# Optimization experiments

Measured on AMD Instinct MI355X. Metric: run time of the kernel, lower is better.

Reference implementation:

```python
import jax, jax.numpy as jnp
import numpy as np

EPS = 1e-5
AVG_D = 32.0


def setup_inputs() -> dict:
    key = jax.random.key(0)
    ks = jax.random.split(key, 12)
    Ns, Nd, E, D, K = 1_000_000, 100_000, 3_200_000, 16, 2
    Fs, Fd, V = 4, 4, 100_000
    F = Fd + K  # predictor fields
    inp = {}
    inp["Cat_src"] = jax.random.randint(ks[0], (Ns, Fs), 0, V)
    inp["Cat_dst"] = jax.random.randint(ks[1], (Nd, Fd), 0, V)
    inp["src_ids"] = jax.random.randint(ks[2], (E,), 0, Ns)
    inp["dst_ids"] = jax.random.randint(ks[3], (E,), 0, Nd)
    inp["label"] = jax.random.randint(ks[4], (Nd,), 0, 2)
    inp["w"] = jax.random.normal(ks[5], (V, D), dtype=jnp.float32) * 0.05
    inp["W_agg"] = jax.random.normal(ks[6], (K, 12 * D, D), dtype=jnp.float32) * 0.05
    inp["b_agg"] = jnp.zeros((K, D), jnp.float32)
    inp["w_lin"] = jax.random.normal(ks[7], (F * D,), dtype=jnp.float32) * 0.05
    inp["b_lin"] = jnp.zeros((1,), jnp.float32)
    inp["W1"] = jax.random.normal(ks[8], (F * D, 64), dtype=jnp.float32) * 0.05
    inp["b1"] = jnp.zeros((64,), jnp.float32)
    inp["W2"] = jax.random.normal(ks[9], (64, 32), dtype=jnp.float32) * 0.05
    inp["b2"] = jnp.zeros((32,), jnp.float32)
    inp["W3"] = jax.random.normal(ks[10], (32, 1), dtype=jnp.float32) * 0.05
    inp["b3"] = jnp.zeros((1,), jnp.float32)
    return inp


def reference(Cat_src, Cat_dst, src_ids, dst_ids, label, w, W_agg, b_agg,
              w_lin, b_lin, W1, b1, W2, b2, W3, b3):
    Nd = Cat_dst.shape[0]
    # --- node embedding: gather cat fields, RowEmb with modes [mean, max] -> [Ns, K, D]
    emb = w[Cat_src]                                      # [Ns, Fs, D]
    h_src = jnp.stack([emb.mean(1), emb.max(1)], axis=1)  # [Ns, K, D]
    # --- multi-aggregator message passing (copy_u + segment min/max/mean, std via mean of h^2)
    m = h_src[src_ids]                                    # [E, K, D]
    deg = jax.ops.segment_sum(jnp.ones(src_ids.shape, m.dtype), dst_ids, Nd)
    safe = jnp.maximum(deg, 1.0)[:, None, None]
    mean = jax.ops.segment_sum(m, dst_ids, Nd) / safe
    mean2 = jax.ops.segment_sum(m * m, dst_ids, Nd) / safe
    has = (deg > 0)[:, None, None]
    mn = jnp.where(has, jax.ops.segment_min(m, dst_ids, Nd), 0.0)
    mx = jnp.where(has, jax.ops.segment_max(m, dst_ids, Nd), 0.0)
    std = jnp.sqrt(jax.nn.relu(mean2 - mean * mean) + EPS)
    tmp = jnp.concatenate([mean, mn, mx, std], axis=-1)   # [Nd, K, 4D]
    # --- PNA degree scalers: identity / amplification / attenuation
    logd = jnp.log(deg + 1.0)
    log_avg = jnp.log(AVG_D + 1.0)
    amp = (logd / log_avg)[:, None, None]
    att = jnp.where(logd > 0, log_avg / jnp.maximum(logd, EPS), 0.0)[:, None, None]
    scaled = jnp.concatenate([tmp, tmp * amp, tmp * att], axis=-1)  # [Nd, K, 12D]
    mes = jnp.einsum('nkf,kfd->nkd', scaled, W_agg) + b_agg          # [Nd, K, D]
    # --- final block: concat dst cat embeddings with aggregated messages
    x = jnp.concatenate([w[Cat_dst], mes], axis=1)        # [Nd, F, D]
    # --- DeepFM predictor: linear + FM pairwise + deep MLP
    flat = x.reshape(Nd, -1)
    lin = flat @ w_lin + b_lin[0]
    s = x.sum(1)
    fm = 0.5 * ((s * s) - (x * x).sum(1)).sum(-1)
    h = jax.nn.relu(flat @ W1 + b1)
    h = jax.nn.relu(h @ W2 + b2)
    deep = (h @ W3 + b3)[:, 0]
    pred = jax.nn.sigmoid(lin + fm + deep)
    return (pred, label)
```

## Files before the change

### kernel.cpp

```cpp
#include <hip/hip_runtime.h>
#include <math.h>

#define EPSF 1e-5f
#define BSH  5
#define BSZ  32
#define MAXB 4096
#define SBH  9
#define MAXSB 256
#define TILE 4096
#define SEG  8
#define BCAP 1472
#define SBCAP (16 * BCAP)
#define XPADS2 104
#define X2PADS 72
#define NPACK 14336

typedef __attribute__((ext_vector_type(8))) short short8;
typedef __attribute__((ext_vector_type(4))) float float4v;

__device__ inline unsigned f2bf_rne(float x) {
    unsigned u = __float_as_uint(x);
    u += 0x7FFF + ((u >> 16) & 1);
    return u >> 16;
}
__device__ inline short bf16_of(float x) { return (short)f2bf_rne(x); }
__device__ inline float bf2f_lo(unsigned hv) { return __uint_as_float(hv << 16); }
__device__ inline float bf2f_hi(unsigned hv) { return __uint_as_float(hv & 0xFFFF0000u); }
__device__ inline float bf2f_s(ushort s) { return __uint_as_float((unsigned)s << 16); }

__global__ __launch_bounds__(256) void setup_all(
    int* sbcursor, int* gcur, int nb, int nsb,
    const float* __restrict__ W_agg, const float* __restrict__ W1,
    const float* __restrict__ W2, ushort* __restrict__ wpack,
    const float* __restrict__ w, ushort* __restrict__ wb, int VD, int do_cast)
{
    int nzc = (nb + 255) >> 8;
    int bid = blockIdx.x;
    if (bid < nzc) {
        int i = bid * 256 + threadIdx.x;
        if (i < nb) gcur[i] = i * BCAP;
        if (i < nsb) sbcursor[i] = i * SBCAP;
        return;
    }
    if (bid == nzc) {
        for (int it = threadIdx.x; it < 1792; it += 256) {
            if (it < 768) {
                int t_g = it >> 6; int rem = it & 63;
                int q = rem >> 4, col = rem & 15;
                int kvar = t_g / 6, t = t_g % 6;
                const float* src = W_agg + kvar * 3072 + (t * 32 + q * 8) * 16 + col;
                ushort* dst = wpack + (size_t)it * 8;
#pragma unroll
                for (int j = 0; j < 8; ++j) dst[j] = (ushort)f2bf_rne(src[j * 16]);
            } else if (it < 1536) {
                int i2 = it - 768;
                int t = i2 >> 8; int rem = i2 & 255;
                int q = rem >> 6, col = rem & 63;
                const float* src = W1 + (t * 32 + q * 8) * 64 + col;
                ushort* dst = wpack + 6144 + (size_t)i2 * 8;
#pragma unroll
                for (int j = 0; j < 8; ++j) dst[j] = (ushort)f2bf_rne(src[j * 64]);
            } else {
                int i2 = it - 1536;
                int t = i2 >> 7; int rem = i2 & 127;
                int q = rem >> 5, col = rem & 31;
                const float* src = W2 + (t * 32 + q * 8) * 32 + col;
                ushort* dst = wpack + 12288 + (size_t)i2 * 8;
#pragma unroll
                for (int j = 0; j < 8; ++j) dst[j] = (ushort)f2bf_rne(src[j * 32]);
            }
        }
        return;
    }
    if (!do_cast) return;
    int i4 = ((bid - nzc - 1) * 256 + threadIdx.x) * 4;
    if (i4 + 3 < VD) {
        float4 v = *(const float4*)(w + i4);
        ushort4 o;
        o.x = (ushort)f2bf_rne(v.x); o.y = (ushort)f2bf_rne(v.y);
        o.z = (ushort)f2bf_rne(v.z); o.w = (ushort)f2bf_rne(v.w);
        *(ushort4*)(wb + i4) = o;
    } else {
        for (int j = i4; j < VD; ++j) wb[j] = (ushort)f2bf_rne(w[j]);
    }
}

__global__ __launch_bounds__(256) void build_h(
    const int* __restrict__ Cat_src, const ushort* __restrict__ wb,
    unsigned* __restrict__ h, int Ns)
{
    int gid = blockIdx.x * 256 + threadIdx.x;
    int s = gid >> 4;
    if (s >= Ns) return;
    int lane = threadIdx.x & 63;
    int d = lane & 15;
    int c = Cat_src[s * 4 + (d & 3)];
    float vs = 0.f, vm = -INFINITY;
#pragma unroll
    for (int f = 0; f < 4; ++f) {
        int id = __shfl(c, (lane & 48) + f, 64);
        float a = bf2f_s(wb[id * 16 + d]);
        vs += a; vm = fmaxf(vm, a);
    }
    unsigned packed = f2bf_rne(vs * 0.25f) | (f2bf_rne(vm) << 16);
    __builtin_nontemporal_store(packed, &h[s * 16 + d]);
}

__global__ __launch_bounds__(256) void scatter_sb(
    const int* __restrict__ src_ids, const int* __restrict__ dst_ids,
    int* sbcursor, unsigned* __restrict__ pairs1, int E, int nsb)
{
    __shared__ int cnt[MAXSB];
    __shared__ int base[MAXSB];
    int tid = threadIdx.x;
    int t0 = blockIdx.x * TILE;
    for (int i = tid; i < nsb; i += 256) cnt[i] = 0;
    __syncthreads();
    int rank[TILE / 256];
#pragma unroll
    for (int j = 0; j < TILE / 256; ++j) {
        int e = t0 + j * 256 + tid;
        rank[j] = (e < E) ? atomicAdd(&cnt[dst_ids[e] >> SBH], 1) : 0;
    }
    __syncthreads();
    for (int i = tid; i < nsb; i += 256) {
        int c = cnt[i];
        base[i] = c ? atomicAdd(&sbcursor[i], c) : 0;
    }
    __syncthreads();
#pragma unroll
    for (int j = 0; j < TILE / 256; ++j) {
        int e = t0 + j * 256 + tid;
        if (e < E) {
            int d = dst_ids[e];
            int sb = d >> SBH;
            int idx = base[sb] + rank[j];
            if (idx < (sb + 1) * SBCAP)
                pairs1[idx] = ((unsigned)src_ids[e] << 9) | (unsigned)(d & 511);
        }
    }
}

__global__ __launch_bounds__(256) void scatter_fine(
    const unsigned* __restrict__ pairs1, const int* __restrict__ sbcursor,
    int* gcur, unsigned* __restrict__ pairs2, int nb, int nsb)
{
    __shared__ int cnt[16];
    __shared__ int base[16];
    int S = blockIdx.x >> 3, seg = blockIdx.x & (SEG - 1);
    int tid = threadIdx.x;
    int sbs = S * SBCAP;
    int sbe = sbcursor[S];
    if (sbe > sbs + SBCAP) sbe = sbs + SBCAP;
    int len = sbe - sbs;
    int per = (len + SEG - 1) / SEG;
    int s0 = sbs + seg * per;
    int s1 = s0 + per; if (s1 > sbe) s1 = sbe;
    if (tid < 16) cnt[tid] = 0;
    __syncthreads();
    int rank[12];
    unsigned pv[12];
    int nit = (s1 - s0 + 255) >> 8;
    if (nit > 12) nit = 12;
    for (int j = 0; j < nit; ++j) {
        int e = s0 + j * 256 + tid;
        if (e < s1) {
            unsigned p = __builtin_nontemporal_load(&pairs1[e]);
            pv[j] = p;
            rank[j] = atomicAdd(&cnt[(p >> 5) & 15], 1);
        }
    }
    __syncthreads();
    if (tid < 16) {
        int gb = (S << 4) + tid;
        int c = cnt[tid];
        base[tid] = (c && gb < nb) ? atomicAdd(&gcur[gb], c) : 0;
    }
    __syncthreads();
    for (int j = 0; j < nit; ++j) {
        int e = s0 + j * 256 + tid;
        if (e < s1) {
            unsigned p = pv[j];
            int fb = (p >> 5) & 15;
            int gb = (S << 4) + fb;
            int idx = base[fb] + rank[j];
            if (idx < (gb + 1) * BCAP)
                pairs2[idx] = p;
        }
    }
}


__device__ inline void bucket_sort(const unsigned* __restrict__ pairs,
                                   int gbase, int cnt,
                                   unsigned* sp, int* hist, int* ofs, int* start,
                                   int tid)
{
    if (tid < BSZ) hist[tid] = 0;
    __syncthreads();
    for (int i = tid; i < cnt; i += 256)
        atomicAdd(&hist[__builtin_nontemporal_load(&pairs[gbase + i]) & (BSZ - 1)], 1);
    __syncthreads();
    if (tid < BSZ) ofs[tid] = hist[tid];
    __syncthreads();
    for (int off = 1; off < BSZ; off <<= 1) {
        int y = (tid < BSZ && tid >= off) ? ofs[tid - off] : 0;
        __syncthreads();
        if (tid < BSZ) ofs[tid] += y;
        __syncthreads();
    }
    if (tid < BSZ) {
        start[tid] = ofs[tid] - hist[tid];
        ofs[tid] = ofs[tid] - hist[tid];
    }
    __syncthreads();
    for (int i = tid; i < cnt; i += 256) {
        unsigned p = __builtin_nontemporal_load(&pairs[gbase + i]);
        int r = atomicAdd(&ofs[p & (BSZ - 1)], 1);
        sp[r] = p;
    }
    __syncthreads();
}

__device__ inline void emit_stats(float sum0, float sq0, float mn0, float mx0,
                                  float sum1, float sq1, float mn1, float mx1,
                                  int dg, int n, int lane, int sub,
                                  ushort* __restrict__ tmpb, int* __restrict__ deg_out)
{
#pragma unroll
    for (int off = 16; off <= 32; off <<= 1) {
        sum0 += __shfl_xor(sum0, off); sq0 += __shfl_xor(sq0, off);
        mn0 = fminf(mn0, __shfl_xor(mn0, off)); mx0 = fmaxf(mx0, __shfl_xor(mx0, off));
        sum1 += __shfl_xor(sum1, off); sq1 += __shfl_xor(sq1, off);
        mn1 = fminf(mn1, __shfl_xor(mn1, off)); mx1 = fmaxf(mx1, __shfl_xor(mx1, off));
    }
    float safe = fmaxf((float)dg, 1.f);
    float r = 1.f / safe;
    bool has = dg > 0;
    float mean0 = sum0 * r, mean1 = sum1 * r;
    float sd0 = sqrtf(fmaxf(sq0 * r - mean0 * mean0, 0.f) + EPSF);
    float sd1 = sqrtf(fmaxf(sq1 * r - mean1 * mean1, 0.f) + EPSF);
    float v0 = (sub == 0) ? mean0 : (sub == 1) ? (has ? mn0 : 0.f)
             : (sub == 2) ? (has ? mx0 : 0.f) : sd0;
    float v1 = (sub == 0) ? mean1 : (sub == 1) ? (has ? mn1 : 0.f)
             : (sub == 2) ? (has ? mx1 : 0.f) : sd1;
    ushort* tp = tmpb + (size_t)n * 128;
    tp[lane] = (ushort)f2bf_rne(v0);
    tp[64 + lane] = (ushort)f2bf_rne(v1);
    if (lane == 0) deg_out[n] = dg;
}

__global__ __launch_bounds__(256) void agg_from_h(
    const unsigned* __restrict__ h, const int* __restrict__ gcur,
    const unsigned* __restrict__ pairs,
    ushort* __restrict__ tmpb, int* __restrict__ deg_out, int Nd)
{
    __shared__ unsigned sp[BCAP];
    __shared__ int hist[BSZ];
    __shared__ int ofs[BSZ];
    __shared__ int start[BSZ];
    int b = blockIdx.x, tid = threadIdx.x;
    int gbase = b * BCAP;
    int cnt = gcur[b] - gbase;
    if (cnt > BCAP) cnt = BCAP;
    if (cnt < 0) cnt = 0;
    bucket_sort(pairs, gbase, cnt, sp, hist, ofs, start, tid);

    int wv = tid >> 6, lane = tid & 63, sub = lane >> 4, d = lane & 15;
#pragma unroll 1
    for (int q = 0; q < 8; ++q) {
        int dl = wv * 8 + q;
        int n = b * BSZ + dl;
        if (n >= Nd) break;
        int st = start[dl], dg = hist[dl];
        float sum0 = 0.f, sq0 = 0.f, mn0 = INFINITY, mx0 = -INFINITY;
        float sum1 = 0.f, sq1 = 0.f, mn1 = INFINITY, mx1 = -INFINITY;
        int nt = (dg + 31) >> 5;
        for (int t = 0; t < nt; ++t) {
            int base = t * 32 + sub;
            unsigned hv[8];
#pragma unroll
            for (int j = 0; j < 8; ++j) {
                int e = base + j * 4;
                int ec = (e < dg) ? e : (dg - 1);
                unsigned p = sp[st + ec];
                hv[j] = h[(p >> 9) * 16 + d];
            }
#pragma unroll
            for (int j = 0; j < 8; ++j) {
                int e = base + j * 4;
                if (e < dg) {
                    float me = bf2f_lo(hv[j]);
                    float vm = bf2f_hi(hv[j]);
                    sum0 += me; sq0 += me * me;
                    mn0 = fminf(mn0, me); mx0 = fmaxf(mx0, me);
                    sum1 += vm; sq1 += vm * vm;
                    mn1 = fminf(mn1, vm); mx1 = fmaxf(mx1, vm);
                }
            }
        }
        emit_stats(sum0, sq0, mn0, mx0, sum1, sq1, mn1, mx1,
                   dg, n, lane, sub, tmpb, deg_out);
    }
}

__global__ __launch_bounds__(256) void agg_from_w(
    const int* __restrict__ Cat_src, const float* __restrict__ w,
    const ushort* __restrict__ wb, int use_bf, const int* __restrict__ gcur,
    const unsigned* __restrict__ pairs,
    ushort* __restrict__ tmpb, int* __restrict__ deg_out, int Nd)
{
    __shared__ unsigned sp[BCAP];
    __shared__ int hist[BSZ];
    __shared__ int ofs[BSZ];
    __shared__ int start[BSZ];
    int b = blockIdx.x, tid = threadIdx.x;
    int gbase = b * BCAP;
    int cnt = gcur[b] - gbase;
    if (cnt > BCAP) cnt = BCAP;
    if (cnt < 0) cnt = 0;
    bucket_sort(pairs, gbase, cnt, sp, hist, ofs, start, tid);

    int wv = tid >> 6, lane = tid & 63, sub = lane >> 4, d = lane & 15;
#pragma unroll 1
    for (int q = 0; q < 8; ++q) {
        int dl = wv * 8 + q;
        int n = b * BSZ + dl;
        if (n >= Nd) break;
        int st = start[dl], dg = hist[dl];
        float sum0 = 0.f, sq0 = 0.f, mn0 = INFINITY, mx0 = -INFINITY;
        float sum1 = 0.f, sq1 = 0.f, mn1 = INFINITY, mx1 = -INFINITY;
        int nt = (dg + 3) >> 2;
        for (int t = 0; t < nt; ++t) {
            int e4 = t * 4 + sub;
            int ec = (e4 < dg) ? e4 : (dg - 1);
            unsigned p = sp[st + ec];
            int src = (int)(p >> 9);
            int cat = Cat_src[src * 4 + (d & 3)];
            float vs = 0.f, vm = -INFINITY;
            if (use_bf) {
#pragma unroll
                for (int f = 0; f < 4; ++f) {
                    int id = __shfl(cat, sub * 16 + f, 64);
                    float a = bf2f_s(wb[id * 16 + d]);
                    vs += a; vm = fmaxf(vm, a);
                }
            } else {
#pragma unroll
                for (int f = 0; f < 4; ++f) {
                    int id = __shfl(cat, sub * 16 + f, 64);
                    float a = w[id * 16 + d];
                    vs += a; vm = fmaxf(vm, a);
                }
            }
            if (e4 < dg) {
                float me = vs * 0.25f;
                sum0 += me; sq0 += me * me;
                mn0 = fminf(mn0, me); mx0 = fmaxf(mx0, me);
                sum1 += vm; sq1 += vm * vm;
                mn1 = fminf(mn1, vm); mx1 = fmaxf(mx1, vm);
            }
        }
        emit_stats(sum0, sq0, mn0, mx0, sum1, sq1, mn1, mx1,
                   dg, n, lane, sub, tmpb, deg_out);
    }
}

__global__ __launch_bounds__(256) void finalize_mfma(
    const int* __restrict__ Cat_dst, const int* __restrict__ label,
    const float* __restrict__ w, const ushort* __restrict__ wpack,
    const float* __restrict__ b_agg,
    const float* __restrict__ w_lin, const float* __restrict__ b_lin,
    const float* __restrict__ b1, const float* __restrict__ b2,
    const float* __restrict__ W3, const float* __restrict__ b3,
    const int* __restrict__ deg_arr, const ushort* __restrict__ tmpb,
    float* __restrict__ out, int Nd)
{
    __shared__ __align__(16) ushort sx[4][16 * XPADS2];
    __shared__ __align__(16) ushort sx2[4][16 * X2PADS];
    __shared__ float sdeep[4][16];

    int tid = threadIdx.x;
    int wv = tid >> 6, lane = tid & 63;
    int q = lane >> 4, m = lane & 15;
    int n0 = (blockIdx.x * 4 + wv) * 16;
    int n = n0 + m;
    int nc = (n < Nd) ? n : (Nd - 1);

    ushort* X = sx[wv];
    ushort* X2 = sx2[wv];

    float fdeg = (float)deg_arr[nc];
    float logd = logf(fdeg + 1.f);
    const float logavg = logf(33.0f);
    float amp = logd / logavg;
    float att = (logd > 0.f) ? (logavg / fmaxf(logd, EPSF)) : 0.f;
    float ampr[4], attr[4];
#pragma unroll
    for (int r = 0; r < 4; ++r) {
        ampr[r] = __shfl(amp, q * 4 + r, 64);
        attr[r] = __shfl(att, q * 4 + r, 64);
    }

    const ushort* tpn = tmpb + (size_t)nc * 128;
#pragma unroll
    for (int kvar = 0; kvar < 2; ++kvar) {
        short8 af0 = *(const short8*)(tpn + kvar * 64 + q * 8);
        short8 af1 = *(const short8*)(tpn + kvar * 64 + 32 + q * 8);
        float4v aI = {0.f,0.f,0.f,0.f}, aA = {0.f,0.f,0.f,0.f}, aT = {0.f,0.f,0.f,0.f};
#pragma unroll
        for (int sb = 0; sb < 3; ++sb) {
            short8 b0 = *(const short8*)(wpack +
                (size_t)(((kvar * 6 + sb * 2) * 4 + q) * 16 + m) * 8);
            short8 b1v = *(const short8*)(wpack +
                (size_t)(((kvar * 6 + sb * 2 + 1) * 4 + q) * 16 + m) * 8);
            if (sb == 0) {
                aI = __builtin_amdgcn_mfma_f32_16x16x32_bf16(af0, b0, aI, 0, 0, 0);
                aI = __builtin_amdgcn_mfma_f32_16x16x32_bf16(af1, b1v, aI, 0, 0, 0);
            } else if (sb == 1) {
                aA = __builtin_amdgcn_mfma_f32_16x16x32_bf16(af0, b0, aA, 0, 0, 0);
                aA = __builtin_amdgcn_mfma_f32_16x16x32_bf16(af1, b1v, aA, 0, 0, 0);
            } else {
                aT = __builtin_amdgcn_mfma_f32_16x16x32_bf16(af0, b0, aT, 0, 0, 0);
                aT = __builtin_amdgcn_mfma_f32_16x16x32_bf16(af1, b1v, aT, 0, 0, 0);
            }
        }
        float bias = b_agg[kvar * 16 + m];
#pragma unroll
        for (int r = 0; r < 4; ++r)
            X[(q * 4 + r) * XPADS2 + 64 + kvar * 16 + m] = (ushort)f2bf_rne(
                aI[r] + ampr[r] * aA[r] + attr[r] * aT[r] + bias);
    }
    {
        int nl = lane >> 2, fl = lane & 3;
        int nn = n0 + nl;
        int nnc = (nn < Nd) ? nn : (Nd - 1);
        int cid = Cat_dst[nnc * 4 + fl];
        const float4* R = (const float4*)(w + (size_t)cid * 16);
        float4 r0 = R[0], r1 = R[1], r2 = R[2], r3 = R[3];
        short8 o0, o1;
        o0[0] = bf16_of(r0.x); o0[1] = bf16_of(r0.y);
        o0[2] = bf16_of(r0.z); o0[3] = bf16_of(r0.w);
        o0[4] = bf16_of(r1.x); o0[5] = bf16_of(r1.y);
        o0[6] = bf16_of(r1.z); o0[7] = bf16_of(r1.w);
        o1[0] = bf16_of(r2.x); o1[1] = bf16_of(r2.y);
        o1[2] = bf16_of(r2.z); o1[3] = bf16_of(r2.w);
        o1[4] = bf16_of(r3.x); o1[5] = bf16_of(r3.y);
        o1[6] = bf16_of(r3.z); o1[7] = bf16_of(r3.w);
        ushort* xp = X + nl * XPADS2 + fl * 16;
        *(short8*)(xp) = o0;
        *(short8*)(xp + 8) = o1;
    }
    __syncthreads();

    float lin = 0.f, sq = 0.f;
    float sd[16];
#pragma unroll
    for (int u = 0; u < 16; ++u) sd[u] = 0.f;
    {
        const ushort* xp = X + m * XPADS2 + q * 16;
        const float* wl = w_lin + q * 16;
#pragma unroll
        for (int u = 0; u < 16; ++u) {
            float v = bf2f_s(xp[u]);
            lin += v * wl[u]; sq += v * v; sd[u] += v;
        }
    }
    if (q < 2) {
        const ushort* xp = X + m * XPADS2 + (4 + q) * 16;
        const float* wl = w_lin + (4 + q) * 16;
#pragma unroll
        for (int u = 0; u < 16; ++u) {
            float v = bf2f_s(xp[u]);
            lin += v * wl[u]; sq += v * v; sd[u] += v;
        }
    }
#pragma unroll
    for (int off = 16; off <= 32; off <<= 1) {
        lin += __shfl_xor(lin, off);
        sq  += __shfl_xor(sq, off);
#pragma unroll
        for (int u = 0; u < 16; ++u) sd[u] += __shfl_xor(sd[u], off);
    }
    float fm = 0.f;
#pragma unroll
    for (int u = 0; u < 16; ++u) fm += sd[u] * sd[u];
    fm = 0.5f * (fm - sq);

    short8 xa[3];
#pragma unroll
    for (int t = 0; t < 3; ++t)
        xa[t] = *(const short8*)(X + m * XPADS2 + t * 32 + q * 8);
#pragma unroll
    for (int nt = 0; nt < 4; ++nt) {
        float4v acc = {0.f, 0.f, 0.f, 0.f};
#pragma unroll
        for (int t = 0; t < 3; ++t) {
            short8 bf = *(const short8*)(wpack + 6144 +
                (size_t)((t * 4 + q) * 64 + nt * 16 + m) * 8);
            acc = __builtin_amdgcn_mfma_f32_16x16x32_bf16(xa[t], bf, acc, 0, 0, 0);
        }
        float bb = b1[nt * 16 + m];
#pragma unroll
        for (int r = 0; r < 4; ++r)
            X2[(q * 4 + r) * X2PADS + nt * 16 + m] =
                (ushort)f2bf_rne(fmaxf(acc[r] + bb, 0.f));
    }
    __syncthreads();

    short8 ha[2];
#pragma unroll
    for (int t = 0; t < 2; ++t)
        ha[t] = *(const short8*)(X2 + m * X2PADS + t * 32 + q * 8);
    float dp[4] = {0.f, 0.f, 0.f, 0.f};
#pragma unroll
    for (int nt = 0; nt < 2; ++nt) {
        float4v acc = {0.f, 0.f, 0.f, 0.f};
#pragma unroll
        for (int t = 0; t < 2; ++t) {
            short8 bf = *(const short8*)(wpack + 12288 +
                (size_t)((t * 4 + q) * 32 + nt * 16 + m) * 8);
            acc = __builtin_amdgcn_mfma_f32_16x16x32_bf16(ha[t], bf, acc, 0, 0, 0);
        }
        float bb = b2[nt * 16 + m];
        float w3 = W3[nt * 16 + m];
#pragma unroll
        for (int r = 0; r < 4; ++r)
            dp[r] += fmaxf(acc[r] + bb, 0.f) * w3;
    }
#pragma unroll
    for (int off = 1; off <= 8; off <<= 1) {
#pragma unroll
        for (int r = 0; r < 4; ++r) dp[r] += __shfl_xor(dp[r], off);
    }
    if (m < 4)
        sdeep[wv][q * 4 + m] = (m == 0) ? dp[0] : (m == 1) ? dp[1]
                             : (m == 2) ? dp[2] : dp[3];
    __syncthreads();
    float deep = sdeep[wv][m];

    if (q == 0 && n < Nd) {
        float z = lin + b_lin[0] + fm + deep + b3[0];
        float pred = 1.f / (1.f + expf(-z));
        out[n] = pred;
        out[Nd + n] = (float)label[n];
    }
}

extern "C" void kernel_launch(void* const* d_in, const int* in_sizes, int n_in,
                              void* d_out, int out_size, void* d_ws, size_t ws_size,
                              hipStream_t stream) {
    const int*   Cat_src = (const int*)d_in[0];
    const int*   Cat_dst = (const int*)d_in[1];
    const int*   src_ids = (const int*)d_in[2];
    const int*   dst_ids = (const int*)d_in[3];
    const int*   label   = (const int*)d_in[4];
    const float* w       = (const float*)d_in[5];
    const float* W_agg   = (const float*)d_in[6];
    const float* b_agg   = (const float*)d_in[7];
    const float* w_lin   = (const float*)d_in[8];
    const float* b_lin   = (const float*)d_in[9];
    const float* W1      = (const float*)d_in[10];
    const float* b1      = (const float*)d_in[11];
    const float* W2      = (const float*)d_in[12];
    const float* b2      = (const float*)d_in[13];
    const float* W3      = (const float*)d_in[14];
    const float* b3      = (const float*)d_in[15];

    int E  = in_sizes[2];
    int Nd = in_sizes[4];
    int Ns = in_sizes[0] / 4;
    int VD = in_sizes[5];
    int nb  = (Nd + BSZ - 1) >> BSH;
    int nsb = (nb + 15) >> 4;

    int* sbcursor = (int*)d_ws;
    int* gcur     = sbcursor + MAXSB;
    int* deg      = gcur + MAXB;
    unsigned* pairs1 = (unsigned*)(deg + Nd);
    unsigned* pairs2 = pairs1 + (size_t)nsb * SBCAP;
    size_t off_tmp = (((size_t)(MAXSB + MAXB + Nd)
                      + (size_t)nsb * SBCAP + (size_t)nb * BCAP) * 4 + 255)
                     & ~(size_t)255;
    ushort* tmpb = (ushort*)((char*)d_ws + off_tmp);
    ushort* wpack = tmpb + (size_t)Nd * 128;
    ushort* w_bf16 = wpack + NPACK;
    unsigned* h  = (unsigned*)(w_bf16 + VD);

    size_t need_common = off_tmp + (size_t)Nd * 256 + (size_t)NPACK * 2;
    size_t need_A = need_common + (size_t)VD * 2;
    size_t need_B = need_A + (size_t)Ns * 64;
    int mode = (ws_size >= need_B) ? 2 : (ws_size >= need_A) ? 1 : 0;

    float* out = (float*)d_out;

    int nzc = (nb + 255) >> 8;
    int ncb = (mode >= 1) ? (VD / 4 + 255) / 256 : 0;
    hipLaunchKernelGGL(setup_all, dim3(nzc + 1 + ncb), dim3(256), 0, stream,
                       sbcursor, gcur, nb, nsb, W_agg, W1, W2, wpack,
                       w, w_bf16, VD, mode >= 1);
    if (mode == 2) {
        int hb = (int)(((size_t)Ns * 16 + 255) / 256);
        hipLaunchKernelGGL(build_h, dim3(hb), dim3(256), 0, stream,
                           Cat_src, w_bf16, h, Ns);
    }
    hipLaunchKernelGGL(scatter_sb, dim3((E + TILE - 1) / TILE), dim3(256), 0, stream,
                       src_ids, dst_ids, sbcursor, pairs1, E, nsb);
    hipLaunchKernelGGL(scatter_fine, dim3(nsb * SEG), dim3(256), 0, stream,
                       pairs1, sbcursor, gcur, pairs2, nb, nsb);
    if (mode == 2) {
        hipLaunchKernelGGL(agg_from_h, dim3(nb), dim3(256), 0, stream,
                           h, gcur, pairs2, tmpb, deg, Nd);
    } else {
        hipLaunchKernelGGL(agg_from_w, dim3(nb), dim3(256), 0, stream,
                           Cat_src, w, w_bf16, mode, gcur, pairs2,
                           tmpb, deg, Nd);
    }
    hipLaunchKernelGGL(finalize_mfma, dim3((Nd + 63) / 64), dim3(256), 0, stream,
                       Cat_dst, label, w, wpack, b_agg, w_lin, b_lin,
                       b1, b2, W3, b3, deg, tmpb, out, Nd);
}
```

Before: 295.7 us.

## Replace two-level bucket scatter with per-destination fixed-capacity slot lists

Measured after the change: 511.6 us. 73.0% more time.

```diff
diff --git a/kernel.cpp b/kernel.cpp
--- a/kernel.cpp
+++ b/kernel.cpp
@@ -2,15 +2,7 @@
 #include <math.h>
 
 #define EPSF 1e-5f
-#define BSH  5
-#define BSZ  32
-#define MAXB 4096
-#define SBH  9
-#define MAXSB 256
-#define TILE 4096
-#define SEG  8
-#define BCAP 1472
-#define SBCAP (16 * BCAP)
+#define CAP  88
 #define XPADS2 104
 #define X2PADS 72
 #define NPACK 14336
@@ -29,17 +21,16 @@
 __device__ inline float bf2f_s(ushort s) { return __uint_as_float((unsigned)s << 16); }
 
 __global__ __launch_bounds__(256) void setup_all(
-    int* sbcursor, int* gcur, int nb, int nsb,
+    int* cnt, int Nd,
     const float* __restrict__ W_agg, const float* __restrict__ W1,
     const float* __restrict__ W2, ushort* __restrict__ wpack,
     const float* __restrict__ w, ushort* __restrict__ wb, int VD, int do_cast)
 {
-    int nzc = (nb + 255) >> 8;
+    int nzc = (Nd + 255) >> 8;
     int bid = blockIdx.x;
     if (bid < nzc) {
         int i = bid * 256 + threadIdx.x;
-        if (i < nb) gcur[i] = i * BCAP;
-        if (i < nsb) sbcursor[i] = i * SBCAP;
+        if (i < Nd) cnt[i] = 0;
         return;
     }
     if (bid == nzc) {
@@ -106,126 +97,36 @@
     __builtin_nontemporal_store(packed, &h[s * 16 + d]);
 }
 
-__global__ __launch_bounds__(256) void scatter_sb(
+__global__ __launch_bounds__(256) void scatter_direct(
     const int* __restrict__ src_ids, const int* __restrict__ dst_ids,
-    int* sbcursor, unsigned* __restrict__ pairs1, int E, int nsb)
-{
-    __shared__ int cnt[MAXSB];
-    __shared__ int base[MAXSB];
-    int tid = threadIdx.x;
-    int t0 = blockIdx.x * TILE;
-    for (int i = tid; i < nsb; i += 256) cnt[i] = 0;
-    __syncthreads();
-    int rank[TILE / 256];
-#pragma unroll
-    for (int j = 0; j < TILE / 256; ++j) {
-        int e = t0 + j * 256 + tid;
-        rank[j] = (e < E) ? atomicAdd(&cnt[dst_ids[e] >> SBH], 1) : 0;
-    }
-    __syncthreads();
-    for (int i = tid; i < nsb; i += 256) {
-        int c = cnt[i];
-        base[i] = c ? atomicAdd(&sbcursor[i], c) : 0;
-    }
-    __syncthreads();
-#pragma unroll
-    for (int j = 0; j < TILE / 256; ++j) {
-        int e = t0 + j * 256 + tid;
-        if (e < E) {
-            int d = dst_ids[e];
-            int sb = d >> SBH;
-            int idx = base[sb] + rank[j];
-            if (idx < (sb + 1) * SBCAP)
-                pairs1[idx] = ((unsigned)src_ids[e] << 9) | (unsigned)(d & 511);
-        }
-    }
-}
-
-__global__ __launch_bounds__(256) void scatter_fine(
-    const unsigned* __restrict__ pairs1, const int* __restrict__ sbcursor,
-    int* gcur, unsigned* __restrict__ pairs2, int nb, int nsb)
-{
-    __shared__ int cnt[16];
-    __shared__ int base[16];
-    int S = blockIdx.x >> 3, seg = blockIdx.x & (SEG - 1);
-    int tid = threadIdx.x;
-    int sbs = S * SBCAP;
-    int sbe = sbcursor[S];
-    if (sbe > sbs + SBCAP) sbe = sbs + SBCAP;
-    int len = sbe - sbs;
-    int per = (len + SEG - 1) / SEG;
-    int s0 = sbs + seg * per;
-    int s1 = s0 + per; if (s1 > sbe) s1 = sbe;
-    if (tid < 16) cnt[tid] = 0;
-    __syncthreads();
-    int rank[12];
-    unsigned pv[12];
-    int nit = (s1 - s0 + 255) >> 8;
-    if (nit > 12) nit = 12;
-    for (int j = 0; j < nit; ++j) {
-        int e = s0 + j * 256 + tid;
-        if (e < s1) {
-            unsigned p = __builtin_nontemporal_load(&pairs1[e]);
-            pv[j] = p;
-            rank[j] = atomicAdd(&cnt[(p >> 5) & 15], 1);
-        }
-    }
-    __syncthreads();
-    if (tid < 16) {
-        int gb = (S << 4) + tid;
-        int c = cnt[tid];
-        base[tid] = (c && gb < nb) ? atomicAdd(&gcur[gb], c) : 0;
-    }
-    __syncthreads();
-    for (int j = 0; j < nit; ++j) {
-        int e = s0 + j * 256 + tid;
-        if (e < s1) {
-            unsigned p = pv[j];
-            int fb = (p >> 5) & 15;
-            int gb = (S << 4) + fb;
-            int idx = base[fb] + rank[j];
-            if (idx < (gb + 1) * BCAP)
-                pairs2[idx] = p;
-        }
-    }
-}
-
-
-__device__ inline void bucket_sort(const unsigned* __restrict__ pairs,
-                                   int gbase, int cnt,
-                                   unsigned* sp, int* hist, int* ofs, int* start,
-                                   int tid)
-{
-    if (tid < BSZ) hist[tid] = 0;
-    __syncthreads();
-    for (int i = tid; i < cnt; i += 256)
-        atomicAdd(&hist[__builtin_nontemporal_load(&pairs[gbase + i]) & (BSZ - 1)], 1);
-    __syncthreads();
-    if (tid < BSZ) ofs[tid] = hist[tid];
-    __syncthreads();
-    for (int off = 1; off < BSZ; off <<= 1) {
-        int y = (tid < BSZ && tid >= off) ? ofs[tid - off] : 0;
-        __syncthreads();
-        if (tid < BSZ) ofs[tid] += y;
-        __syncthreads();
-    }
-    if (tid < BSZ) {
-        start[tid] = ofs[tid] - hist[tid];
-        ofs[tid] = ofs[tid] - hist[tid];
-    }
-    __syncthreads();
-    for (int i = tid; i < cnt; i += 256) {
-        unsigned p = __builtin_nontemporal_load(&pairs[gbase + i]);
-        int r = atomicAdd(&ofs[p & (BSZ - 1)], 1);
-        sp[r] = p;
-    }
-    __syncthreads();
+    int* __restrict__ cnt, unsigned* __restrict__ pairs, int E)
+{
+    int i = blockIdx.x * 256 + threadIdx.x;
+    int e0 = i * 4;
+    if (e0 + 3 < E) {
+        int4 s  = *(const int4*)(src_ids + e0);
+        int4 dd = *(const int4*)(dst_ids + e0);
+        int sl0 = atomicAdd(&cnt[dd.x], 1);
+        int sl1 = atomicAdd(&cnt[dd.y], 1);
+        int sl2 = atomicAdd(&cnt[dd.z], 1);
+        int sl3 = atomicAdd(&cnt[dd.w], 1);
+        if (sl0 < CAP) pairs[(size_t)dd.x * CAP + sl0] = (unsigned)s.x;
+        if (sl1 < CAP) pairs[(size_t)dd.y * CAP + sl1] = (unsigned)s.y;
+        if (sl2 < CAP) pairs[(size_t)dd.z * CAP + sl2] = (unsigned)s.z;
+        if (sl3 < CAP) pairs[(size_t)dd.w * CAP + sl3] = (unsigned)s.w;
+    } else {
+        for (int e = e0; e < E; ++e) {
+            int dd = dst_ids[e];
+            int sl = atomicAdd(&cnt[dd], 1);
+            if (sl < CAP) pairs[(size_t)dd * CAP + sl] = (unsigned)src_ids[e];
+        }
+    }
 }
 
 __device__ inline void emit_stats(float sum0, float sq0, float mn0, float mx0,
                                   float sum1, float sq1, float mn1, float mx1,
                                   int dg, int n, int lane, int sub,
-                                  ushort* __restrict__ tmpb, int* __restrict__ deg_out)
+                                  ushort* __restrict__ tmpb)
 {
 #pragma unroll
     for (int off = 16; off <= 32; off <<= 1) {
@@ -247,49 +148,61 @@
     ushort* tp = tmpb + (size_t)n * 128;
     tp[lane] = (ushort)f2bf_rne(v0);
     tp[64 + lane] = (ushort)f2bf_rne(v1);
-    if (lane == 0) deg_out[n] = dg;
-}
-
-__global__ __launch_bounds__(256) void agg_from_h(
-    const unsigned* __restrict__ h, const int* __restrict__ gcur,
+}
+
+__global__ __launch_bounds__(256) void agg_from_h2(
+    const unsigned* __restrict__ h, const int* __restrict__ cnt,
     const unsigned* __restrict__ pairs,
-    ushort* __restrict__ tmpb, int* __restrict__ deg_out, int Nd)
-{
-    __shared__ unsigned sp[BCAP];
-    __shared__ int hist[BSZ];
-    __shared__ int ofs[BSZ];
-    __shared__ int start[BSZ];
-    int b = blockIdx.x, tid = threadIdx.x;
-    int gbase = b * BCAP;
-    int cnt = gcur[b] - gbase;
-    if (cnt > BCAP) cnt = BCAP;
-    if (cnt < 0) cnt = 0;
-    bucket_sort(pairs, gbase, cnt, sp, hist, ofs, start, tid);
-
+    ushort* __restrict__ tmpb, int Nd)
+{
+    int tid = threadIdx.x;
     int wv = tid >> 6, lane = tid & 63, sub = lane >> 4, d = lane & 15;
-#pragma unroll 1
-    for (int q = 0; q < 8; ++q) {
-        int dl = wv * 8 + q;
-        int n = b * BSZ + dl;
-        if (n >= Nd) break;
-        int st = start[dl], dg = hist[dl];
-        float sum0 = 0.f, sq0 = 0.f, mn0 = INFINITY, mx0 = -INFINITY;
-        float sum1 = 0.f, sq1 = 0.f, mn1 = INFINITY, mx1 = -INFINITY;
-        int nt = (dg + 31) >> 5;
-        for (int t = 0; t < nt; ++t) {
-            int base = t * 32 + sub;
-            unsigned hv[8];
-#pragma unroll
-            for (int j = 0; j < 8; ++j) {
-                int e = base + j * 4;
-                int ec = (e < dg) ? e : (dg - 1);
-                unsigned p = sp[st + ec];
-                hv[j] = h[(p >> 9) * 16 + d];
+    int n = blockIdx.x * 4 + wv;
+    if (n >= Nd) return;
+    int dg = cnt[n];
+    int dgc = (dg < CAP) ? dg : CAP;
+    const unsigned* pw = pairs + (size_t)n * CAP;
+
+    float sum0 = 0.f, sq0 = 0.f, mn0 = INFINITY, mx0 = -INFINITY;
+    float sum1 = 0.f, sq1 = 0.f, mn1 = INFINITY, mx1 = -INFINITY;
+
+    int nfull = dgc >> 5;
+    for (int t = 0; t < nfull; ++t) {
+        const unsigned* pp = pw + t * 32 + sub;
+        unsigned pv[8], hv[8];
+#pragma unroll
+        for (int j = 0; j < 8; ++j) pv[j] = pp[j * 4];
+#pragma unroll
+        for (int j = 0; j < 8; ++j) hv[j] = h[pv[j] * 16 + d];
+#pragma unroll
+        for (int j = 0; j < 8; ++j) {
+            float me = bf2f_lo(hv[j]);
+            float vm = bf2f_hi(hv[j]);
+            sum0 += me; sq0 += me * me;
+            mn0 = fminf(mn0, me); mx0 = fmaxf(mx0, me);
+            sum1 += vm; sq1 += vm * vm;
+            mn1 = fminf(mn1, vm); mx1 = fmaxf(mx1, vm);
+        }
+    }
+    int base = nfull << 5;
+    int rem = dgc - base;
+    if (rem > 0) {
+        int last = dgc - 1;
+        unsigned pv[8], hv[8];
+#pragma unroll
+        for (int j = 0; j < 8; ++j) {
+            if (j * 4 < rem) {
+                int e = base + j * 4 + sub;
+                pv[j] = pw[e < last ? e : last];
             }
-#pragma unroll
-            for (int j = 0; j < 8; ++j) {
-                int e = base + j * 4;
-                if (e < dg) {
+        }
+#pragma unroll
+        for (int j = 0; j < 8; ++j)
+            if (j * 4 < rem) hv[j] = h[pv[j] * 16 + d];
+#pragma unroll
+        for (int j = 0; j < 8; ++j) {
+            if (j * 4 < rem) {
+                if (base + j * 4 + sub < dgc) {
                     float me = bf2f_lo(hv[j]);
                     float vm = bf2f_hi(hv[j]);
                     sum0 += me; sq0 += me * me;
@@ -299,71 +212,59 @@
                 }
             }
         }
-        emit_stats(sum0, sq0, mn0, mx0, sum1, sq1, mn1, mx1,
-                   dg, n, lane, sub, tmpb, deg_out);
-    }
-}
-
-__global__ __launch_bounds__(256) void agg_from_w(
+    }
+    emit_stats(sum0, sq0, mn0, mx0, sum1, sq1, mn1, mx1,
+               dg, n, lane, sub, tmpb);
+}
+
+__global__ __launch_bounds__(256) void agg_from_w2(
     const int* __restrict__ Cat_src, const float* __restrict__ w,
-    const ushort* __restrict__ wb, int use_bf, const int* __restrict__ gcur,
-    const unsigned* __restrict__ pairs,
-    ushort* __restrict__ tmpb, int* __restrict__ deg_out, int Nd)
-{
-    __shared__ unsigned sp[BCAP];
-    __shared__ int hist[BSZ];
-    __shared__ int ofs[BSZ];
-    __shared__ int start[BSZ];
-    int b = blockIdx.x, tid = threadIdx.x;
-    int gbase = b * BCAP;
-    int cnt = gcur[b] - gbase;
-    if (cnt > BCAP) cnt = BCAP;
-    if (cnt < 0) cnt = 0;
-    bucket_sort(pairs, gbase, cnt, sp, hist, ofs, start, tid);
-
+    const ushort* __restrict__ wb, int use_bf,
+    const int* __restrict__ cnt, const unsigned* __restrict__ pairs,
+    ushort* __restrict__ tmpb, int Nd)
+{
+    int tid = threadIdx.x;
     int wv = tid >> 6, lane = tid & 63, sub = lane >> 4, d = lane & 15;
-#pragma unroll 1
-    for (int q = 0; q < 8; ++q) {
-        int dl = wv * 8 + q;
-        int n = b * BSZ + dl;
-        if (n >= Nd) break;
-        int st = start[dl], dg = hist[dl];
-        float sum0 = 0.f, sq0 = 0.f, mn0 = INFINITY, mx0 = -INFINITY;
-        float sum1 = 0.f, sq1 = 0.f, mn1 = INFINITY, mx1 = -INFINITY;
-        int nt = (dg + 3) >> 2;
-        for (int t = 0; t < nt; ++t) {
-            int e4 = t * 4 + sub;
-            int ec = (e4 < dg) ? e4 : (dg - 1);
-            unsigned p = sp[st + ec];
-            int src = (int)(p >> 9);
-            int cat = Cat_src[src * 4 + (d & 3)];
-            float vs = 0.f, vm = -INFINITY;
-            if (use_bf) {
-#pragma unroll
-                for (int f = 0; f < 4; ++f) {
-                    int id = __shfl(cat, sub * 16 + f, 64);
-                    float a = bf2f_s(wb[id * 16 + d]);
-                    vs += a; vm = fmaxf(vm, a);
-                }
-            } else {
-#pragma unroll
-                for (int f = 0; f < 4; ++f) {
-                    int id = __shfl(cat, sub * 16 + f, 64);
-                    float a = w[id * 16 + d];
-                    vs += a; vm = fmaxf(vm, a);
-                }
+    int n = blockIdx.x * 4 + wv;
+    if (n >= Nd) return;
+    int dg = cnt[n];
+    int dgc = (dg < CAP) ? dg : CAP;
+    const unsigned* pw = pairs + (size_t)n * CAP;
+
+    float sum0 = 0.f, sq0 = 0.f, mn0 = INFINITY, mx0 = -INFINITY;
+    float sum1 = 0.f, sq1 = 0.f, mn1 = INFINITY, mx1 = -INFINITY;
+    int nt = (dgc + 3) >> 2;
+    for (int t = 0; t < nt; ++t) {
+        int e4 = t * 4 + sub;
+        int ec = (e4 < dgc) ? e4 : (dgc - 1);
+        int src = (int)pw[ec];
+        int cat = Cat_src[src * 4 + (d & 3)];
+        float vs = 0.f, vm = -INFINITY;
+        if (use_bf) {
+#pragma unroll
+            for (int f = 0; f < 4; ++f) {
+                int id = __shfl(cat, sub * 16 + f, 64);
+                float a = bf2f_s(wb[id * 16 + d]);
+                vs += a; vm = fmaxf(vm, a);
             }
-            if (e4 < dg) {
-                float me = vs * 0.25f;
-                sum0 += me; sq0 += me * me;
-                mn0 = fminf(mn0, me); mx0 = fmaxf(mx0, me);
-                sum1 += vm; sq1 += vm * vm;
-                mn1 = fminf(mn1, vm); mx1 = fmaxf(mx1, vm);
+        } else {
+#pragma unroll
+            for (int f = 0; f < 4; ++f) {
+                int id = __shfl(cat, sub * 16 + f, 64);
+                float a = w[id * 16 + d];
+                vs += a; vm = fmaxf(vm, a);
             }
         }
-        emit_stats(sum0, sq0, mn0, mx0, sum1, sq1, mn1, mx1,
-                   dg, n, lane, sub, tmpb, deg_out);
-    }
+        if (e4 < dgc) {
+            float me = vs * 0.25f;
+            sum0 += me; sq0 += me * me;
+            mn0 = fminf(mn0, me); mx0 = fmaxf(mx0, me);
+            sum1 += vm; sq1 += vm * vm;
+            mn1 = fminf(mn1, vm); mx1 = fmaxf(mx1, vm);
+        }
+    }
+    emit_stats(sum0, sq0, mn0, mx0, sum1, sq1, mn1, mx1,
+               dg, n, lane, sub, tmpb);
 }
 
 __global__ __launch_bounds__(256) void finalize_mfma(
@@ -571,17 +472,10 @@
     int Nd = in_sizes[4];
     int Ns = in_sizes[0] / 4;
     int VD = in_sizes[5];
-    int nb  = (Nd + BSZ - 1) >> BSH;
-    int nsb = (nb + 15) >> 4;
-
-    int* sbcursor = (int*)d_ws;
-    int* gcur     = sbcursor + MAXSB;
-    int* deg      = gcur + MAXB;
-    unsigned* pairs1 = (unsigned*)(deg + Nd);
-    unsigned* pairs2 = pairs1 + (size_t)nsb * SBCAP;
-    size_t off_tmp = (((size_t)(MAXSB + MAXB + Nd)
-                      + (size_t)nsb * SBCAP + (size_t)nb * BCAP) * 4 + 255)
-                     & ~(size_t)255;
+
+    int* cnt = (int*)d_ws;
+    unsigned* pairs = (unsigned*)(cnt + Nd);
+    size_t off_tmp = (((size_t)Nd + (size_t)Nd * CAP) * 4 + 255) & ~(size_t)255;
     ushort* tmpb = (ushort*)((char*)d_ws + off_tmp);
     ushort* wpack = tmpb + (size_t)Nd * 128;
     ushort* w_bf16 = wpack + NPACK;
@@ -594,29 +488,27 @@
 
     float* out = (float*)d_out;
 
-    int nzc = (nb + 255) >> 8;
+    int nzc = (Nd + 255) >> 8;
     int ncb = (mode >= 1) ? (VD / 4 + 255) / 256 : 0;
     hipLaunchKernelGGL(setup_all, dim3(nzc + 1 + ncb), dim3(256), 0, stream,
-                       sbcursor, gcur, nb, nsb, W_agg, W1, W2, wpack,
-                       w, w_bf16, VD, mode >= 1);
+                       cnt, Nd, W_agg, W1, W2, wpack, w, w_bf16, VD, mode >= 1);
     if (mode == 2) {
         int hb = (int)(((size_t)Ns * 16 + 255) / 256);
         hipLaunchKernelGGL(build_h, dim3(hb), dim3(256), 0, stream,
                            Cat_src, w_bf16, h, Ns);
     }
-    hipLaunchKernelGGL(scatter_sb, dim3((E + TILE - 1) / TILE), dim3(256), 0, stream,
-                       src_ids, dst_ids, sbcursor, pairs1, E, nsb);
-    hipLaunchKernelGGL(scatter_fine, dim3(nsb * SEG), dim3(256), 0, stream,
-                       pairs1, sbcursor, gcur, pairs2, nb, nsb);
+    int nth = (E + 3) >> 2;
+    hipLaunchKernelGGL(scatter_direct, dim3((nth + 255) >> 8), dim3(256), 0, stream,
+                       src_ids, dst_ids, cnt, pairs, E);
+    int nab = (Nd + 3) >> 2;
     if (mode == 2) {
-        hipLaunchKernelGGL(agg_from_h, dim3(nb), dim3(256), 0, stream,
-                           h, gcur, pairs2, tmpb, deg, Nd);
+        hipLaunchKernelGGL(agg_from_h2, dim3(nab), dim3(256), 0, stream,
+                           h, cnt, pairs, tmpb, Nd);
     } else {
-        hipLaunchKernelGGL(agg_from_w, dim3(nb), dim3(256), 0, stream,
-                           Cat_src, w, w_bf16, mode, gcur, pairs2,
-                           tmpb, deg, Nd);
+        hipLaunchKernelGGL(agg_from_w2, dim3(nab), dim3(256), 0, stream,
+                           Cat_src, w, w_bf16, mode, cnt, pairs, tmpb, Nd);
     }
     hipLaunchKernelGGL(finalize_mfma, dim3((Nd + 63) / 64), dim3(256), 0, stream,
                        Cat_dst, label, w, wpack, b_agg, w_lin, b_lin,
-                       b1, b2, W3, b3, deg, tmpb, out, Nd);
-}
+                       b1, b2, W3, b3, cnt, tmpb, out, Nd);
+}
```
